# Kernel optimization log

Measured on AMD Instinct MI355X. Metric: run time of the kernel, lower is better.

## Reference

```python
import jax, jax.numpy as jnp
import numpy as np

H = 4096      # hidden_size
NH = 32       # num heads
HD = H // NH  # head_dim = 128
I = 11008     # intermediate_size
T = 1024      # prompt tokens
G = 128       # AWQ group size
EPS = 1e-6
ROPE_BASE = 10000.0


def _pack4(key, in_f, out_f):
    # pack 8 uint4 nibbles per int32, [in_f, out_f/8]
    nib = jax.random.randint(key, (in_f, out_f // 8, 8), 0, 16, dtype=jnp.int32)
    shifts = (jnp.arange(8, dtype=jnp.int32) * 4)
    return jnp.bitwise_or.reduce(nib << shifts, axis=-1).astype(jnp.int32)


def _dequant(qw, qz, sc):
    # qw:[in,out/8] int32, qz:[in/G,out/8] int32, sc:[in/G,out] float
    shifts = jnp.arange(8, dtype=jnp.int32) * 4
    w = ((qw[:, :, None] >> shifts) & 0xF).reshape(qw.shape[0], -1)   # [in,out]
    z = ((qz[:, :, None] >> shifts) & 0xF).reshape(qz.shape[0], -1)   # [groups,out]
    gidx = jnp.arange(qw.shape[0]) // G
    return (w.astype(sc.dtype) - z.astype(sc.dtype)[gidx]) * sc[gidx]


def _qlinear(x, qw, qz, sc):
    return x @ _dequant(qw, qz, sc)


def _rmsnorm(x, w):
    var = jnp.mean(x * x, axis=-1, keepdims=True)
    return x * jax.lax.rsqrt(var + EPS) * w


def _rope(x, positions):
    # x: [T, NH, HD], neox-style half rotation (vLLM rotary)
    inv = 1.0 / (ROPE_BASE ** (jnp.arange(0, HD, 2, dtype=jnp.float32) / HD))
    freqs = positions.astype(jnp.float32)[:, None] * inv[None, :]     # [T, HD/2]
    cos = jnp.cos(freqs)[:, None, :]
    sin = jnp.sin(freqs)[:, None, :]
    x1, x2 = jnp.split(x, 2, axis=-1)
    return jnp.concatenate([x1 * cos - x2 * sin, x2 * cos + x1 * sin], axis=-1)


def _attention(positions, q, k, v):
    # causal self-attention over the prompt (prefill writes k/v to cache then attends)
    q = _rope(q.reshape(T, NH, HD), positions)
    k = _rope(k.reshape(T, NH, HD), positions)
    v = v.reshape(T, NH, HD)
    scale = HD ** -0.5
    scores = jnp.einsum('qhd,khd->hqk', q, k) * scale
    mask = jnp.tril(jnp.ones((T, T), dtype=bool))
    scores = jnp.where(mask[None], scores, jnp.finfo(scores.dtype).min)
    probs = jax.nn.softmax(scores, axis=-1)
    out = jnp.einsum('hqk,khd->qhd', probs, v)
    return out.reshape(T, NH * HD)


def setup_inputs() -> dict:
    key = jax.random.key(0)
    ks = jax.random.split(key, 16)
    S = 0.002  # AWQ scale magnitude
    inp = {
        'positions': jnp.arange(T, dtype=jnp.int32),
        'hidden_states': jax.random.normal(ks[0], (T, H), dtype=jnp.float32),
        'ln1_w': jnp.ones((H,), dtype=jnp.float32),
        'ln2_w': jnp.ones((H,), dtype=jnp.float32),
        'qkv_qw': _pack4(ks[1], H, 3 * H),
        'qkv_qz': _pack4(ks[2], H // G, 3 * H),
        'qkv_sc': jax.random.uniform(ks[3], (H // G, 3 * H), dtype=jnp.float32) * S,
        'o_qw': _pack4(ks[4], H, H),
        'o_qz': _pack4(ks[5], H // G, H),
        'o_sc': jax.random.uniform(ks[6], (H // G, H), dtype=jnp.float32) * S,
        'gate_qw': _pack4(ks[7], H, I),
        'gate_qz': _pack4(ks[8], H // G, I),
        'gate_sc': jax.random.uniform(ks[9], (H // G, I), dtype=jnp.float32) * S,
        'up_qw': _pack4(ks[10], H, I),
        'up_qz': _pack4(ks[11], H // G, I),
        'up_sc': jax.random.uniform(ks[12], (H // G, I), dtype=jnp.float32) * S,
        'down_qw': _pack4(ks[13], I, H),
        'down_qz': _pack4(ks[14], I // G, H),
        'down_sc': jax.random.uniform(ks[15], (I // G, H), dtype=jnp.float32) * S,
    }
    return inp


def reference(positions, hidden_states, ln1_w, qkv_qw, qkv_qz, qkv_sc,
              o_qw, o_qz, o_sc, gate_qw, gate_qz, gate_sc,
              up_qw, up_qz, up_sc, down_qw, down_qz, down_sc, ln2_w):
    # --- self attention block ---
    residual = hidden_states
    x = _rmsnorm(hidden_states, ln1_w)
    qkv = _qlinear(x, qkv_qw, qkv_qz, qkv_sc)                # [T, 3H]
    q, k, v = jnp.split(qkv, 3, axis=-1)
    attn_out = _attention(positions, q, k, v)                # [T, H]
    x = _qlinear(attn_out, o_qw, o_qz, o_sc)
    hidden = residual + x
    # --- MLP block ---
    residual = hidden
    x = _rmsnorm(hidden, ln2_w)
    gate = jax.nn.silu(_qlinear(x, gate_qw, gate_qz, gate_sc))
    up = _qlinear(x, up_qw, up_qz, up_sc)
    x = _qlinear(gate * up, down_qw, down_qz, down_sc)
    return residual + x
```

## Files before the change

kernel.cpp:

```cpp
#include <hip/hip_runtime.h>
#include <cstdint>

typedef __attribute__((ext_vector_type(8))) short  bf16x8;
typedef __attribute__((ext_vector_type(4))) float  f32x4;
typedef __attribute__((ext_vector_type(4))) unsigned int uint4v;
typedef __attribute__((ext_vector_type(2))) unsigned int uint2v;

typedef const __attribute__((address_space(1))) void* gas_t;
typedef __attribute__((address_space(3))) void* las_t;

__device__ __forceinline__ float bf2f(unsigned short b) {
    union { unsigned int u; float f; } v; v.u = ((unsigned int)b) << 16; return v.f;
}
__device__ __forceinline__ unsigned short f2bf(float f) {
    union { float f; unsigned int u; } v; v.f = f;
    unsigned int r = v.u + 0x7FFFu + ((v.u >> 16) & 1u);
    return (unsigned short)(r >> 16);
}
__device__ __forceinline__ float u2f(unsigned int u) {
    union { unsigned int u; float f; } v; v.u = u; return v.f;
}

__global__ __launch_bounds__(256)
void dequant_kernel(const int* __restrict__ qw, const int* __restrict__ qz,
                    const float* __restrict__ sc, unsigned short* __restrict__ out,
                    int NW, int K)
{
    const int t   = threadIdx.x;
    const int wcb = blockIdx.x << 5;
    const int kb  = blockIdx.y << 6;
    const int g   = blockIdx.y >> 1;
    const int N   = NW << 3;
    const int wc  = wcb + (t >> 3);
    const int k0  = kb + ((t & 7) << 3);

    unsigned int w[8];
#pragma unroll
    for (int j = 0; j < 8; j++) w[j] = (unsigned int)qw[(size_t)(k0 + j) * NW + wc];
    const unsigned int zw = (unsigned int)qz[(size_t)g * NW + wc];
    float scv[8];
#pragma unroll
    for (int j2 = 0; j2 < 8; j2++) scv[j2] = sc[(size_t)g * N + (wc << 3) + j2];

#pragma unroll
    for (int j2 = 0; j2 < 8; j2++) {
        const int sh = j2 << 2;
        const float s = scv[j2];
        const float moff = -(8388608.0f + (float)((zw >> sh) & 0xFu)) * s;
        unsigned int pk[4];
#pragma unroll
        for (int i = 0; i < 4; i++) {
            float f0 = fmaf(u2f(((w[2*i]   >> sh) & 0xFu) | 0x4B000000u), s, moff);
            float f1 = fmaf(u2f(((w[2*i+1] >> sh) & 0xFu) | 0x4B000000u), s, moff);
            asm("v_cvt_pk_bf16_f32 %0, %1, %2" : "=v"(pk[i]) : "v"(f0), "v"(f1));
        }
        uint4v ov = {pk[0], pk[1], pk[2], pk[3]};
        *(uint4v*)(out + (size_t)((wc << 3) + j2) * K + k0) = ov;
    }
}

__global__ __launch_bounds__(256)
void rmsnorm_kernel(const float* __restrict__ x, const float* __restrict__ wgt,
                    unsigned short* __restrict__ out)
{
    const int t = blockIdx.x, tid = threadIdx.x;
    const float4* xr = (const float4*)(x + (size_t)t * 4096);
    float4 v[4];
    float ss = 0.f;
#pragma unroll
    for (int j = 0; j < 4; j++) {
        v[j] = xr[(j << 8) + tid];
        ss += v[j].x*v[j].x + v[j].y*v[j].y + v[j].z*v[j].z + v[j].w*v[j].w;
    }
#pragma unroll
    for (int m = 1; m < 64; m <<= 1) ss += __shfl_xor(ss, m);
    __shared__ float red[4];
    if ((tid & 63) == 0) red[tid >> 6] = ss;
    __syncthreads();
    float tot = red[0] + red[1] + red[2] + red[3];
    float rs = rsqrtf(tot * (1.f / 4096.f) + 1e-6f);
    const float4* wr = (const float4*)wgt;
#pragma unroll
    for (int j = 0; j < 4; j++) {
        float4 wv = wr[(j << 8) + tid];
        float4 xv = v[j];
        unsigned int p0 = (unsigned int)f2bf(xv.x*rs*wv.x) | ((unsigned int)f2bf(xv.y*rs*wv.y) << 16);
        unsigned int p1 = (unsigned int)f2bf(xv.z*rs*wv.z) | ((unsigned int)f2bf(xv.w*rs*wv.w) << 16);
        uint2v pk = {p0, p1};
        *(uint2v*)(&out[(size_t)t*4096 + (size_t)(((j << 8) + tid) << 2)]) = pk;
    }
}

template<int MODE>
__global__ __launch_bounds__(256, 4)
void bt_gemm(const unsigned short* __restrict__ A,
             const unsigned short* __restrict__ Bt0,
             const unsigned short* __restrict__ Bt1,
             void* __restrict__ out0, void* __restrict__ out1,
             const float* __restrict__ res,
             int N, int K, int NB)
{
    const int flat = blockIdx.x;
    const int work = NB * (flat & 7) + (flat >> 3);
    const int n0 = (work >> 3) << 7;
    const int m0 = (work & 7) << 7;

    const unsigned short* Bt = Bt0;
    void* outp = out0;
    if (MODE == 1 && blockIdx.z == 1) { Bt = Bt1; outp = out1; }

    __shared__ unsigned short As[128 * 64];
    __shared__ unsigned short Bs[128 * 64];

    const int tid  = threadIdx.x;
    const int lane = tid & 63;
    const int wid  = tid >> 6;
    const int wm   = wid >> 1, wn = wid & 1;

    f32x4 acc[4][4];
#pragma unroll
    for (int i = 0; i < 4; i++)
#pragma unroll
        for (int j = 0; j < 4; j++) { f32x4 zv = {0.f,0.f,0.f,0.f}; acc[i][j] = zv; }

    const int nsteps = K >> 6;
    for (int t = 0; t < nsteps; t++) {
        const int k0 = t << 6;
        __syncthreads();
#pragma unroll
        for (int i = 0; i < 4; i++) {
            int slot = (i << 8) + tid;
            int row = slot >> 3, s = slot & 7;
            __builtin_amdgcn_global_load_lds(
                (gas_t)(A + (size_t)(m0 + row) * K + k0 + ((s ^ (row & 7)) << 3)),
                (las_t)&As[slot << 3], 16, 0, 0);
        }
#pragma unroll
        for (int i = 0; i < 4; i++) {
            int slot = (i << 8) + tid;
            int row = slot >> 3, s = slot & 7;
            __builtin_amdgcn_global_load_lds(
                (gas_t)(Bt + (size_t)(n0 + row) * K + k0 + ((s ^ (row & 7)) << 3)),
                (las_t)&Bs[slot << 3], 16, 0, 0);
        }
        __syncthreads();
#pragma unroll
        for (int kk = 0; kk < 2; kk++) {
            const int srow = (kk << 2) + (lane >> 4);
            bf16x8 af[4], bfv[4];
#pragma unroll
            for (int mi = 0; mi < 4; mi++) {
                int r = (wm << 6) + (mi << 4) + (lane & 15);
                af[mi] = *(const bf16x8*)(&As[(r << 6) + ((srow ^ (r & 7)) << 3)]);
            }
#pragma unroll
            for (int ni = 0; ni < 4; ni++) {
                int r = (wn << 6) + (ni << 4) + (lane & 15);
                bfv[ni] = *(const bf16x8*)(&Bs[(r << 6) + ((srow ^ (r & 7)) << 3)]);
            }
#pragma unroll
            for (int mi = 0; mi < 4; mi++)
#pragma unroll
                for (int ni = 0; ni < 4; ni++)
                    acc[mi][ni] = __builtin_amdgcn_mfma_f32_16x16x32_bf16(af[mi], bfv[ni], acc[mi][ni], 0, 0, 0);
        }
    }

    const int rbase = m0 + (wm << 6) + ((lane >> 4) << 2);
    const int cbase = n0 + (wn << 6) + (lane & 15);
#pragma unroll
    for (int mi = 0; mi < 4; mi++) {
#pragma unroll
        for (int r = 0; r < 4; r++) {
            int row = rbase + (mi << 4) + r;
#pragma unroll
            for (int ni = 0; ni < 4; ni++) {
                int col = cbase + (ni << 4);
                float v = acc[mi][ni][r];
                if (MODE == 3) {
                    ((float*)out0)[(size_t)row * N + col] = v + res[(size_t)row * N + col];
                } else {
                    ((unsigned short*)outp)[(size_t)row * N + col] = f2bf(v);
                }
            }
        }
    }
}

__global__ __launch_bounds__(256)
void rope_kernel(const int* __restrict__ positions, const unsigned short* __restrict__ qkv,
                 unsigned short* __restrict__ Qr, unsigned short* __restrict__ Kr,
                 unsigned short* __restrict__ Vtp)
{
    const int t = blockIdx.x, tid = threadIdx.x;
    const float p = (float)positions[t];
    const unsigned short* row = qkv + (size_t)t * 12288;
#pragma unroll 4
    for (int it = 0; it < 16; it++) {
        int task = (it << 8) + tid;
        int i   = task & 63;
        int hh  = (task >> 6) & 31;
        int isK = task >> 11;
        float fr = p * __expf(-(float)i * 0.14391156831f);
        float s, c;
        __sincosf(fr, &s, &c);
        const unsigned short* src = row + (isK << 12) + (hh << 7);
        float x1 = bf2f(src[i]);
        float x2 = bf2f(src[64 + i]);
        float o1 = x1 * c - x2 * s;
        float o2 = x2 * c + x1 * s;
        if (!isK) { o1 *= 0.08838834764831845f; o2 *= 0.08838834764831845f; }
        unsigned short* dst = (isK ? Kr : Qr) + ((size_t)hh * 1024 + t) * 128;
        dst[i]      = f2bf(o1);
        dst[64 + i] = f2bf(o2);
    }
#pragma unroll 4
    for (int it = 0; it < 16; it++) {
        int task = (it << 8) + tid;
        int d = task & 127, hh = task >> 7;
        Vtp[((size_t)hh * 128 + d) * 1024 + t] = row[8192 + task];
    }
}

__global__ __launch_bounds__(256, 2)
void attn_kernel(const unsigned short* __restrict__ Qr, const unsigned short* __restrict__ Kr,
                 const unsigned short* __restrict__ Vtp, unsigned short* __restrict__ attn_out)
{
    __shared__ unsigned short Ks[64 * 128];
    __shared__ unsigned short Vs[128 * 64];
    __shared__ unsigned short Ps[4][16 * 64];
    const int tid = threadIdx.x, lane = tid & 63, w = tid >> 6;
    const int qt = blockIdx.x, h = blockIdx.y;

    const unsigned short* Qh = Qr + ((size_t)h * 1024 + (size_t)qt * 64) * 128;

    bf16x8 qf[4];
#pragma unroll
    for (int kk = 0; kk < 4; kk++)
        qf[kk] = *(const bf16x8*)(Qh + (size_t)((w << 4) + (lane & 15)) * 128 + (kk << 5) + ((lane >> 4) << 3));

    f32x4 o[8];
#pragma unroll
    for (int i = 0; i < 8; i++) { f32x4 zf = {0.f,0.f,0.f,0.f}; o[i] = zf; }
    float Mr[4] = {-1e30f, -1e30f, -1e30f, -1e30f};
    float Lr[4] = {0.f, 0.f, 0.f, 0.f};
    const int qrow0 = (qt << 6) + (w << 4) + ((lane >> 4) << 2);

    for (int kt = 0; kt <= qt; kt++) {
        __syncthreads();
#pragma unroll
        for (int j = 0; j < 4; j++) {
            int slot = (j << 8) + tid;
            int rw = slot >> 4, s = slot & 15;
            int ssrc = (s & 8) | ((s ^ (rw & 7)) & 7);
            const uint4v* src = (const uint4v*)(Kr + ((size_t)h * 1024 + (size_t)kt * 64 + rw) * 128 + (ssrc << 3));
            *(uint4v*)(&Ks[(rw << 7) + (s << 3)]) = *src;
        }
#pragma unroll
        for (int j = 0; j < 4; j++) {
            int slot = (j << 8) + tid;
            int rw = slot >> 3, s = slot & 7;
            const uint4v* src = (const uint4v*)(Vtp + ((size_t)h * 128 + rw) * 1024 + (kt << 6) + ((s ^ (rw & 7)) << 3));
            *(uint4v*)(&Vs[(rw << 6) + (s << 3)]) = *src;
        }
        __syncthreads();

        f32x4 sc4[4];
#pragma unroll
        for (int ni = 0; ni < 4; ni++) { f32x4 zf = {0.f,0.f,0.f,0.f}; sc4[ni] = zf; }
#pragma unroll
        for (int kk = 0; kk < 4; kk++) {
#pragma unroll
            for (int ni = 0; ni < 4; ni++) {
                int r = (ni << 4) + (lane & 15);
                int s = (kk << 2) + (lane >> 4);
                int sp = (s & 8) | ((s ^ (r & 7)) & 7);
                bf16x8 kf = *(const bf16x8*)(&Ks[(r << 7) + (sp << 3)]);
                sc4[ni] = __builtin_amdgcn_mfma_f32_16x16x32_bf16(qf[kk], kf, sc4[ni], 0, 0, 0);
            }
        }

#pragma unroll
        for (int r = 0; r < 4; r++) {
            int qg = qrow0 + r;
            float mx = -1e30f;
#pragma unroll
            for (int ni = 0; ni < 4; ni++) {
                int kg_ = (kt << 6) + (ni << 4) + (lane & 15);
                float v = sc4[ni][r];
                if (kt == qt && kg_ > qg) { v = -1e30f; sc4[ni][r] = v; }
                mx = fmaxf(mx, v);
            }
#pragma unroll
            for (int m_ = 1; m_ < 16; m_ <<= 1) mx = fmaxf(mx, __shfl_xor(mx, m_));
            float mnew  = fmaxf(Mr[r], mx);
            float alpha = __expf(Mr[r] - mnew);
            Mr[r] = mnew;
            float rs = 0.f;
#pragma unroll
            for (int ni = 0; ni < 4; ni++) {
                float pv = __expf(sc4[ni][r] - mnew);
                sc4[ni][r] = pv;
                rs += pv;
            }
#pragma unroll
            for (int m_ = 1; m_ < 16; m_ <<= 1) rs += __shfl_xor(rs, m_);
            Lr[r] = Lr[r] * alpha + rs;
#pragma unroll
            for (int nd = 0; nd < 8; nd++) o[nd][r] *= alpha;
        }

#pragma unroll
        for (int r = 0; r < 4; r++) {
            int qr = ((lane >> 4) << 2) + r;
#pragma unroll
            for (int ni = 0; ni < 4; ni++) {
                int col = (ni << 4) + (lane & 15);
                int phys = (col >> 3) ^ (qr & 7);
                Ps[w][(qr << 6) + (phys << 3) + (col & 7)] = f2bf(sc4[ni][r]);
            }
        }
#pragma unroll
        for (int kk2 = 0; kk2 < 2; kk2++) {
            int rowp = lane & 15;
            int sl = (kk2 << 2) + (lane >> 4);
            bf16x8 pa = *(const bf16x8*)(&Ps[w][(rowp << 6) + ((sl ^ (rowp & 7)) << 3)]);
#pragma unroll
            for (int nd = 0; nd < 8; nd++) {
                int rv = (nd << 4) + (lane & 15);
                bf16x8 vb = *(const bf16x8*)(&Vs[(rv << 6) + ((sl ^ (rv & 7)) << 3)]);
                o[nd] = __builtin_amdgcn_mfma_f32_16x16x32_bf16(pa, vb, o[nd], 0, 0, 0);
            }
        }
    }

#pragma unroll
    for (int r = 0; r < 4; r++) {
        float inv = 1.0f / Lr[r];
        int trow = qrow0 + r;
#pragma unroll
        for (int nd = 0; nd < 8; nd++) {
            int col = (h << 7) + (nd << 4) + (lane & 15);
            attn_out[(size_t)trow * 4096 + col] = f2bf(o[nd][r] * inv);
        }
    }
}

__global__ __launch_bounds__(256)
void silu_mul_kernel(const unsigned short* __restrict__ gate, unsigned short* __restrict__ up)
{
    size_t idx = ((size_t)blockIdx.x * 256 + threadIdx.x) * 8;
    uint4v g = *(const uint4v*)(gate + idx);
    uint4v u = *(const uint4v*)(up + idx);
    unsigned int outp[4];
#pragma unroll
    for (int j = 0; j < 4; j++) {
        unsigned int gw = g[j], uw = u[j];
        float g0 = bf2f((unsigned short)(gw & 0xFFFF)), g1 = bf2f((unsigned short)(gw >> 16));
        float u0 = bf2f((unsigned short)(uw & 0xFFFF)), u1 = bf2f((unsigned short)(uw >> 16));
        float s0 = g0 / (1.f + __expf(-g0)) * u0;
        float s1 = g1 / (1.f + __expf(-g1)) * u1;
        outp[j] = (unsigned int)f2bf(s0) | ((unsigned int)f2bf(s1) << 16);
    }
    uint4v ov = {outp[0], outp[1], outp[2], outp[3]};
    *(uint4v*)(up + idx) = ov;
}

extern "C" void kernel_launch(void* const* d_in, const int* in_sizes, int n_in,
                              void* d_out, int out_size, void* d_ws, size_t ws_size,
                              hipStream_t stream)
{
    const int*   positions = (const int*)  d_in[0];
    const float* hidden    = (const float*)d_in[1];
    const float* ln1       = (const float*)d_in[2];
    const float* ln2       = (const float*)d_in[3];
    const int*   qkv_qw    = (const int*)  d_in[4];
    const int*   qkv_qz    = (const int*)  d_in[5];
    const float* qkv_sc    = (const float*)d_in[6];
    const int*   o_qw      = (const int*)  d_in[7];
    const int*   o_qz      = (const int*)  d_in[8];
    const float* o_sc      = (const float*)d_in[9];
    const int*   gate_qw   = (const int*)  d_in[10];
    const int*   gate_qz   = (const int*)  d_in[11];
    const float* gate_sc   = (const float*)d_in[12];
    const int*   up_qw     = (const int*)  d_in[13];
    const int*   up_qz     = (const int*)  d_in[14];
    const float* up_sc     = (const float*)d_in[15];
    const int*   down_qw   = (const int*)  d_in[16];
    const int*   down_qz   = (const int*)  d_in[17];
    const float* down_sc   = (const float*)d_in[18];

    char* ws = (char*)d_ws;
    const size_t MB = 1 << 20;
    unsigned short* Wt    = (unsigned short*)(ws + 0);
    unsigned short* Wu    = (unsigned short*)(ws + 86 * MB);
    unsigned short* xln   = (unsigned short*)(ws + 176 * MB);
    unsigned short* qkvb  = (unsigned short*)(ws + 184 * MB);
    unsigned short* Qrp   = (unsigned short*)(ws + 208 * MB);
    unsigned short* Krp   = (unsigned short*)(ws + 216 * MB);
    unsigned short* Vtp   = (unsigned short*)(ws + 224 * MB);
    unsigned short* attnb = (unsigned short*)(ws + 232 * MB);
    float*          hid   = (float*)        (ws + 240 * MB);
    unsigned short* x2    = xln;
    unsigned short* gateb = qkvb;
    unsigned short* upb   = Qrp;

    dequant_kernel<<<dim3(48, 64), 256, 0, stream>>>(qkv_qw, qkv_qz, qkv_sc, Wt, 1536, 4096);
    rmsnorm_kernel<<<1024, 256, 0, stream>>>(hidden, ln1, xln);
    bt_gemm<0><<<768, 256, 0, stream>>>(xln, Wt, nullptr,
                                        (void*)qkvb, nullptr, nullptr, 12288, 4096, 96);
    rope_kernel<<<1024, 256, 0, stream>>>(positions, qkvb, Qrp, Krp, Vtp);
    dequant_kernel<<<dim3(16, 64), 256, 0, stream>>>(o_qw, o_qz, o_sc, Wt, 512, 4096);
    attn_kernel<<<dim3(16, 32), 256, 0, stream>>>(Qrp, Krp, Vtp, attnb);
    bt_gemm<3><<<256, 256, 0, stream>>>(attnb, Wt, nullptr,
                                        (void*)hid, nullptr, hidden, 4096, 4096, 32);
    rmsnorm_kernel<<<1024, 256, 0, stream>>>(hid, ln2, x2);
    dequant_kernel<<<dim3(43, 64), 256, 0, stream>>>(gate_qw, gate_qz, gate_sc, Wt, 1376, 4096);
    dequant_kernel<<<dim3(43, 64), 256, 0, stream>>>(up_qw, up_qz, up_sc, Wu, 1376, 4096);
    bt_gemm<1><<<dim3(688, 1, 2), 256, 0, stream>>>(x2, Wt, Wu,
                                                    (void*)gateb, (void*)upb, nullptr,
                                                    11008, 4096, 86);
    silu_mul_kernel<<<5504, 256, 0, stream>>>(gateb, upb);
    dequant_kernel<<<dim3(16, 172), 256, 0, stream>>>(down_qw, down_qz, down_sc, Wt, 512, 11008);
    bt_gemm<3><<<256, 256, 0, stream>>>(upb, Wt, nullptr,
                                        d_out, nullptr, hid, 4096, 11008, 32);
}
```

Before: 749.1 us.

## Co-schedule weight dequant with GEMMs and split-K the down projection

Result: faster. 685.8 us (-8.5%).

```diff
diff --git a/kernel.cpp b/kernel.cpp
--- a/kernel.cpp
+++ b/kernel.cpp
@@ -21,15 +21,14 @@
     union { unsigned int u; float f; } v; v.u = u; return v.f;
 }
 
-__global__ __launch_bounds__(256)
-void dequant_kernel(const int* __restrict__ qw, const int* __restrict__ qz,
-                    const float* __restrict__ sc, unsigned short* __restrict__ out,
-                    int NW, int K)
-{
-    const int t   = threadIdx.x;
-    const int wcb = blockIdx.x << 5;
-    const int kb  = blockIdx.y << 6;
-    const int g   = blockIdx.y >> 1;
+__device__ __forceinline__ void dequant_block(int bx, int by, int t,
+    const int* __restrict__ qw, const int* __restrict__ qz,
+    const float* __restrict__ sc, unsigned short* __restrict__ out,
+    int NW, int K)
+{
+    const int wcb = bx << 5;
+    const int kb  = by << 6;
+    const int g   = by >> 1;
     const int N   = NW << 3;
     const int wc  = wcb + (t >> 3);
     const int k0  = kb + ((t & 7) << 3);
@@ -57,6 +56,14 @@
         uint4v ov = {pk[0], pk[1], pk[2], pk[3]};
         *(uint4v*)(out + (size_t)((wc << 3) + j2) * K + k0) = ov;
     }
+}
+
+__global__ __launch_bounds__(256)
+void dequant_kernel(const int* __restrict__ qw, const int* __restrict__ qz,
+                    const float* __restrict__ sc, unsigned short* __restrict__ out,
+                    int NW, int K)
+{
+    dequant_block(blockIdx.x, blockIdx.y, threadIdx.x, qw, qz, sc, out, NW, K);
 }
 
 __global__ __launch_bounds__(256)
@@ -98,16 +105,37 @@
              const unsigned short* __restrict__ Bt1,
              void* __restrict__ out0, void* __restrict__ out1,
              const float* __restrict__ res,
-             int N, int K, int NB)
+             int N, int K, int NB, int gemmBlocks, int ksplit,
+             const int* dq1_qw, const int* dq1_qz, const float* dq1_sc,
+             unsigned short* dq1_out, int dq1_NW, int dq1_K, int dq1_blocks,
+             const int* dq2_qw, const int* dq2_qz, const float* dq2_sc,
+             unsigned short* dq2_out, int dq2_NW, int dq2_K)
 {
     const int flat = blockIdx.x;
+    if (flat >= gemmBlocks) {
+        if (blockIdx.z != 0) return;
+        int db = flat - gemmBlocks;
+        if (db < dq1_blocks) {
+            int xb = dq1_NW >> 5;
+            dequant_block(db % xb, db / xb, threadIdx.x, dq1_qw, dq1_qz, dq1_sc, dq1_out, dq1_NW, dq1_K);
+        } else {
+            db -= dq1_blocks;
+            int xb = dq2_NW >> 5;
+            dequant_block(db % xb, db / xb, threadIdx.x, dq2_qw, dq2_qz, dq2_sc, dq2_out, dq2_NW, dq2_K);
+        }
+        return;
+    }
+
     const int work = NB * (flat & 7) + (flat >> 3);
     const int n0 = (work >> 3) << 7;
     const int m0 = (work & 7) << 7;
+    const int z  = blockIdx.z;
 
     const unsigned short* Bt = Bt0;
     void* outp = out0;
-    if (MODE == 1 && blockIdx.z == 1) { Bt = Bt1; outp = out1; }
+    if (MODE == 1 && z == 1) { Bt = Bt1; outp = out1; }
+    const int k0base = (MODE == 2) ? z * ksplit : 0;
+    const int nsteps = ((MODE == 2) ? ksplit : K) >> 6;
 
     __shared__ unsigned short As[128 * 64];
     __shared__ unsigned short Bs[128 * 64];
@@ -123,9 +151,8 @@
 #pragma unroll
         for (int j = 0; j < 4; j++) { f32x4 zv = {0.f,0.f,0.f,0.f}; acc[i][j] = zv; }
 
-    const int nsteps = K >> 6;
     for (int t = 0; t < nsteps; t++) {
-        const int k0 = t << 6;
+        const int k0 = k0base + (t << 6);
         __syncthreads();
 #pragma unroll
         for (int i = 0; i < 4; i++) {
@@ -179,12 +206,36 @@
                 float v = acc[mi][ni][r];
                 if (MODE == 3) {
                     ((float*)out0)[(size_t)row * N + col] = v + res[(size_t)row * N + col];
+                } else if (MODE == 2) {
+                    ((unsigned short*)out0)[(size_t)z * ((size_t)1024 * N) + (size_t)row * N + col] = f2bf(v);
                 } else {
                     ((unsigned short*)outp)[(size_t)row * N + col] = f2bf(v);
                 }
             }
         }
     }
+}
+
+__global__ __launch_bounds__(256)
+void reduce2_kernel(const float* __restrict__ base, const unsigned short* __restrict__ part,
+                    float* __restrict__ out)
+{
+    const size_t i = (size_t)blockIdx.x * 256 + threadIdx.x;
+    const size_t stride = (size_t)1024 * 4096;
+    float s[8];
+    float4 a0 = ((const float4*)base)[2*i], a1 = ((const float4*)base)[2*i+1];
+    s[0]=a0.x; s[1]=a0.y; s[2]=a0.z; s[3]=a0.w; s[4]=a1.x; s[5]=a1.y; s[6]=a1.z; s[7]=a1.w;
+#pragma unroll
+    for (int p = 0; p < 2; p++) {
+        uint4v v = *(const uint4v*)(part + p * stride + i * 8);
+#pragma unroll
+        for (int j = 0; j < 4; j++) {
+            s[2*j]   += bf2f((unsigned short)(v[j] & 0xFFFF));
+            s[2*j+1] += bf2f((unsigned short)(v[j] >> 16));
+        }
+    }
+    float4 o0 = {s[0],s[1],s[2],s[3]}, o1 = {s[4],s[5],s[6],s[7]};
+    ((float4*)out)[2*i] = o0; ((float4*)out)[2*i+1] = o1;
 }
 
 __global__ __launch_bounds__(256)
@@ -347,8 +398,18 @@
 }
 
 __global__ __launch_bounds__(256)
-void silu_mul_kernel(const unsigned short* __restrict__ gate, unsigned short* __restrict__ up)
-{
+void silu_deq_kernel(const unsigned short* __restrict__ gate, unsigned short* __restrict__ up,
+                     int siluBlocks,
+                     const int* __restrict__ qw, const int* __restrict__ qz,
+                     const float* __restrict__ sc, unsigned short* __restrict__ wout,
+                     int NW, int K)
+{
+    if (blockIdx.x >= siluBlocks) {
+        int db = blockIdx.x - siluBlocks;
+        int xb = NW >> 5;
+        dequant_block(db % xb, db / xb, threadIdx.x, qw, qz, sc, wout, NW, K);
+        return;
+    }
     size_t idx = ((size_t)blockIdx.x * 256 + threadIdx.x) * 8;
     uint4v g = *(const uint4v*)(gate + idx);
     uint4v u = *(const uint4v*)(up + idx);
@@ -392,36 +453,48 @@
 
     char* ws = (char*)d_ws;
     const size_t MB = 1 << 20;
-    unsigned short* Wt    = (unsigned short*)(ws + 0);
-    unsigned short* Wu    = (unsigned short*)(ws + 86 * MB);
-    unsigned short* xln   = (unsigned short*)(ws + 176 * MB);
-    unsigned short* qkvb  = (unsigned short*)(ws + 184 * MB);
-    unsigned short* Qrp   = (unsigned short*)(ws + 208 * MB);
-    unsigned short* Krp   = (unsigned short*)(ws + 216 * MB);
-    unsigned short* Vtp   = (unsigned short*)(ws + 224 * MB);
-    unsigned short* attnb = (unsigned short*)(ws + 232 * MB);
-    float*          hid   = (float*)        (ws + 240 * MB);
-    unsigned short* x2    = xln;
-    unsigned short* gateb = qkvb;
-    unsigned short* upb   = Qrp;
-
-    dequant_kernel<<<dim3(48, 64), 256, 0, stream>>>(qkv_qw, qkv_qz, qkv_sc, Wt, 1536, 4096);
+    unsigned short* W_qkv = (unsigned short*)(ws + 0);
+    unsigned short* Qrp   = (unsigned short*)(ws + 0);
+    unsigned short* Krp   = (unsigned short*)(ws + 8 * MB);
+    unsigned short* Vtp   = (unsigned short*)(ws + 16 * MB);
+    unsigned short* W_gate= (unsigned short*)(ws + 0);
+    unsigned short* W_down= (unsigned short*)(ws + 0);
+    unsigned short* attnb = (unsigned short*)(ws + 86 * MB);
+    unsigned short* W_o   = (unsigned short*)(ws + 96 * MB);
+    unsigned short* gateb = (unsigned short*)(ws + 96 * MB);
+    unsigned short* part  = (unsigned short*)(ws + 96 * MB);
+    unsigned short* W_up  = (unsigned short*)(ws + 128 * MB);
+    unsigned short* xln   = (unsigned short*)(ws + 214 * MB);
+    unsigned short* qkvb  = (unsigned short*)(ws + 222 * MB);
+    unsigned short* upb   = (unsigned short*)(ws + 222 * MB);
+    float*          hid   = (float*)d_out;
+
+    dequant_kernel<<<dim3(48, 64), 256, 0, stream>>>(qkv_qw, qkv_qz, qkv_sc, W_qkv, 1536, 4096);
     rmsnorm_kernel<<<1024, 256, 0, stream>>>(hidden, ln1, xln);
-    bt_gemm<0><<<768, 256, 0, stream>>>(xln, Wt, nullptr,
-                                        (void*)qkvb, nullptr, nullptr, 12288, 4096, 96);
+    bt_gemm<0><<<768 + 1024 + 2752, 256, 0, stream>>>(
+        xln, W_qkv, nullptr, (void*)qkvb, nullptr, nullptr,
+        12288, 4096, 96, 768, 0,
+        o_qw, o_qz, o_sc, W_o, 512, 4096, 1024,
+        up_qw, up_qz, up_sc, W_up, 1376, 4096);
     rope_kernel<<<1024, 256, 0, stream>>>(positions, qkvb, Qrp, Krp, Vtp);
-    dequant_kernel<<<dim3(16, 64), 256, 0, stream>>>(o_qw, o_qz, o_sc, Wt, 512, 4096);
     attn_kernel<<<dim3(16, 32), 256, 0, stream>>>(Qrp, Krp, Vtp, attnb);
-    bt_gemm<3><<<256, 256, 0, stream>>>(attnb, Wt, nullptr,
-                                        (void*)hid, nullptr, hidden, 4096, 4096, 32);
-    rmsnorm_kernel<<<1024, 256, 0, stream>>>(hid, ln2, x2);
-    dequant_kernel<<<dim3(43, 64), 256, 0, stream>>>(gate_qw, gate_qz, gate_sc, Wt, 1376, 4096);
-    dequant_kernel<<<dim3(43, 64), 256, 0, stream>>>(up_qw, up_qz, up_sc, Wu, 1376, 4096);
-    bt_gemm<1><<<dim3(688, 1, 2), 256, 0, stream>>>(x2, Wt, Wu,
-                                                    (void*)gateb, (void*)upb, nullptr,
-                                                    11008, 4096, 86);
-    silu_mul_kernel<<<5504, 256, 0, stream>>>(gateb, upb);
-    dequant_kernel<<<dim3(16, 172), 256, 0, stream>>>(down_qw, down_qz, down_sc, Wt, 512, 11008);
-    bt_gemm<3><<<256, 256, 0, stream>>>(upb, Wt, nullptr,
-                                        d_out, nullptr, hid, 4096, 11008, 32);
-}
+    bt_gemm<3><<<256 + 2752, 256, 0, stream>>>(
+        attnb, W_o, nullptr, (void*)hid, nullptr, hidden,
+        4096, 4096, 32, 256, 0,
+        gate_qw, gate_qz, gate_sc, W_gate, 1376, 4096, 2752,
+        nullptr, nullptr, nullptr, nullptr, 32, 64);
+    rmsnorm_kernel<<<1024, 256, 0, stream>>>(hid, ln2, xln);
+    bt_gemm<1><<<dim3(688, 1, 2), 256, 0, stream>>>(
+        xln, W_gate, W_up, (void*)gateb, (void*)upb, nullptr,
+        11008, 4096, 86, 688, 0,
+        nullptr, nullptr, nullptr, nullptr, 32, 64, 0,
+        nullptr, nullptr, nullptr, nullptr, 32, 64);
+    silu_deq_kernel<<<5504 + 2752, 256, 0, stream>>>(
+        gateb, upb, 5504, down_qw, down_qz, down_sc, W_down, 512, 11008);
+    bt_gemm<2><<<dim3(256, 1, 2), 256, 0, stream>>>(
+        upb, W_down, nullptr, (void*)part, nullptr, nullptr,
+        4096, 11008, 32, 256, 5504,
+        nullptr, nullptr, nullptr, nullptr, 32, 64, 0,
+        nullptr, nullptr, nullptr, nullptr, 32, 64);
+    reduce2_kernel<<<2048, 256, 0, stream>>>(hid, part, (float*)d_out);
+}
```
